# Kernel tuning notes

Hardware: AMD Instinct MI355X
Metric: run time of the kernel (lower is better)

The kernel has to match this reference:

```python
import jax, jax.numpy as jnp
from jax import lax
import numpy as np

NUM_TAGS = 128
BATCH = 256
SEQ = 1024


def setup_inputs() -> dict:
    key = jax.random.key(0)
    k1, k2, k3 = jax.random.split(key, 3)
    emissions = jax.random.normal(k1, (BATCH, SEQ, NUM_TAGS), dtype=jnp.float32)
    tags = jax.random.randint(k2, (BATCH, SEQ), 0, NUM_TAGS)
    mask = jnp.ones((BATCH, SEQ), dtype=jnp.float32)
    # xavier_uniform on [K,K] then clamp to [-1,1]
    limit = float(np.sqrt(6.0 / (NUM_TAGS + NUM_TAGS)))
    transitions = jnp.clip(
        jax.random.uniform(k3, (NUM_TAGS, NUM_TAGS), minval=-limit, maxval=limit),
        -1.0, 1.0).astype(jnp.float32)
    return {"emissions": emissions, "transitions": transitions, "tags": tags, "mask": mask}


def _log_partition(emissions, transitions, mask):
    # emissions: [B,S,K], mask: [B,S]
    alpha0 = emissions[:, 0]  # [B,K]
    emit_ts = jnp.swapaxes(emissions[:, 1:], 0, 1)  # [S-1,B,K]
    mask_ts = jnp.swapaxes(mask[:, 1:], 0, 1)       # [S-1,B]

    def step(alpha, xs):
        emit_t, mask_t = xs
        # [B,K,1] + [1,K,K] + [B,1,K] -> logsumexp over prev-tag axis
        new = jax.nn.logsumexp(alpha[:, :, None] + transitions[None, :, :] + emit_t[:, None, :], axis=1)
        alpha = jnp.where(mask_t[:, None].astype(bool), new, alpha)
        return alpha, None

    alpha, _ = lax.scan(step, alpha0, (emit_ts, mask_ts))
    return jax.nn.logsumexp(alpha, axis=1)  # [B]


def reference(emissions, transitions, tags, mask):
    # gold-path score
    emit_score = jnp.take_along_axis(emissions, tags[:, :, None], axis=2)[:, :, 0]  # [B,S]
    score = (emit_score * mask).sum(axis=1)
    trans_scores = transitions[tags[:, :-1], tags[:, 1:]] * mask[:, 1:]
    score = score + trans_scores.sum(axis=1)
    logZ = _log_partition(emissions, transitions, mask)
    return (logZ - score).mean()
```

## Files before the change

kernel.cpp:

```cpp
#include <hip/hip_runtime.h>
#include <stdint.h>

#define SEQ      1024
#define NT       128
#define NBATCH   256
#define MID      512
#define WS_STRIDE 132

#if defined(__has_builtin)
#if __has_builtin(__builtin_amdgcn_fdot2_f32_bf16)
#define HAVE_BF16_DOT2 1
#endif
#endif

#ifdef HAVE_BF16_DOT2
typedef __bf16 v2bf __attribute__((ext_vector_type(2)));
#define DOT2ACC(a, su, wu) \
    a = __builtin_amdgcn_fdot2_f32_bf16(__builtin_bit_cast(v2bf, (su)), \
                                        __builtin_bit_cast(v2bf, (wu)), a, false)
#else
#define DOT2ACC(a, su, wu) { \
    a = fmaf(__uint_as_float((wu) << 16),         __uint_as_float((su) << 16),         a); \
    a = fmaf(__uint_as_float((wu) & 0xffff0000u), __uint_as_float((su) & 0xffff0000u), a); }
#endif

#define RALL(X) X(0) X(1) X(2) X(3) X(4) X(5) X(6) X(7) \
                X(8) X(9) X(10) X(11) X(12) X(13) X(14) X(15)
#define DECLW(k) uint32_t W##k;
#define INITW(k) { \
    float f0_ = __expf(wbase[(2 * (k)    ) * wstr]); \
    float f1_ = __expf(wbase[(2 * (k) + 1) * wstr]); \
    asm("v_cvt_pk_bf16_f32 %0, %1, %2" : "=v"(W##k) : "v"(f0_), "v"(f1_)); }
#define PINW(k)  asm volatile("" : "+v"(W##k));

#define MQ(c, k0, k1, k2, k3) { \
    uint4 u_ = *(const uint4*)(gp + 4 * (c)); \
    DOT2ACC(a0, u_.x, W##k0); \
    DOT2ACC(a1, u_.y, W##k1); \
    DOT2ACC(a2, u_.z, W##k2); \
    DOT2ACC(a3, u_.w, W##k3); }

#define MATVEC32(S_) { \
    float a0 = 0.f, a1 = 0.f, a2 = 0.f, a3 = 0.f; \
    MQ(0,0,1,2,3) MQ(1,4,5,6,7) MQ(2,8,9,10,11) MQ(3,12,13,14,15) \
    S_ = (a0 + a1) + (a2 + a3); \
    S_ += __shfl_xor(S_, 1, 64); \
    S_ += __shfl_xor(S_, 2, 64); }

#define BF16_STORE(buf_, val_) { \
    uint32_t pk_; \
    asm("v_cvt_pk_bf16_f32 %0, %1, %2" : "=v"(pk_) : "v"(val_), "v"(val_)); \
    ((unsigned short*)(buf_))[jt] = (unsigned short)(pk_ & 0xffffu); }

__global__ __launch_bounds__(512) void crf_chains(
    const float* __restrict__ emissions,
    const float* __restrict__ transitions,
    const int*   __restrict__ tags,
    const float* __restrict__ mask,
    float* __restrict__ out,
    float* __restrict__ ws)
{
    const int blk = blockIdx.x;
    const int tid = threadIdx.x;

    if (blk >= 2 * NBATCH) {
        int b    = (blk - 2 * NBATCH) * 8 + (tid >> 6);
        int lane = tid & 63;
        const float* emb = emissions + (size_t)b * SEQ * NT;
        const int*   tgb = tags + (size_t)b * SEQ;
        const float* mkb = mask + (size_t)b * SEQ;
        float sc = 0.f;
        for (int t = lane; t < SEQ; t += 64) {
            int   tg = tgb[t];
            float mt = mkb[t];
            sc += emb[t * NT + tg] * mt;
            if (t >= 1) sc += transitions[tgb[t - 1] * NT + tg] * mt;
        }
#pragma unroll
        for (int o = 32; o > 0; o >>= 1) sc += __shfl_down(sc, o, 64);
        if (lane == 0) atomicAdd(out, -sc * (1.0f / NBATCH));
        return;
    }

    __shared__ __align__(16) uint32_t buf[2][NT / 2];

    const int jt = tid >> 2;
    const int q  = tid & 3;

    const bool fwd = (blk < NBATCH);
    const int  b   = fwd ? blk : blk - NBATCH;

    const float* emb = emissions + (size_t)b * SEQ * NT;
    const float* mkb = mask + (size_t)b * SEQ;

    const float* wbase = fwd ? (transitions + (size_t)(32 * q) * NT + jt)
                             : (transitions + (size_t)jt * NT + 32 * q);
    const int    wstr  = fwd ? NT : 1;

    RALL(DECLW)
    RALL(INITW)
    RALL(PINW)

    int   kSum = 0, p = 0;
    float gcur = 0.f, beta = 1.0f;
    float E0, E1, M0, M1;

    if (fwd) {
        gcur = __expf(emb[jt]);
        if (q == 0) BF16_STORE(buf[0], gcur);
        E0 = emb[1 * NT + jt];  E1 = emb[2 * NT + jt];
        M0 = mkb[1];            M1 = mkb[2];
    } else {
        float w0 = __expf(emb[(size_t)(SEQ - 1) * NT + jt]);
        if (q == 0) BF16_STORE(buf[0], w0);
        E0 = emb[(size_t)(SEQ - 2) * NT + jt];
        E1 = emb[(size_t)(SEQ - 3) * NT + jt];
        M0 = mkb[SEQ - 1];      M1 = mkb[SEQ - 2];
    }
    __syncthreads();

    if (fwd) {
        for (int s = 0; s < MID; ++s) {
            float En = emb[(size_t)(3 + s) * NT + jt];
            float Mn = mkb[3 + s];
            if (M0 != 0.0f) {
                const uint32_t* gp = buf[p] + 16 * q;
                uint32_t anchor = buf[p][0];
                float sres;
                MATVEC32(sres);
                int   e  = (int)((anchor >> 7) & 0xff);
                float rc = __uint_as_float((uint32_t)(254 - e) << 23);
                kSum += e - 127;
                if (q == 0) {
                    gcur = sres * rc * __expf(E0);
                    BF16_STORE(buf[p ^ 1], gcur);
                }
                p ^= 1;
            }
            __syncthreads();
            E0 = E1; E1 = En; M0 = M1; M1 = Mn;
        }
        float* wsb = ws + (size_t)b * WS_STRIDE;
        if (q == 0)  wsb[jt] = gcur;
        if (tid == 0) wsb[128] = (float)kSum;
    } else {
        for (int s = 0; s < MID - 1; ++s) {
            float En = emb[(size_t)(SEQ - 4 - s) * NT + jt];
            float Mn = mkb[SEQ - 3 - s];
            {
                const uint32_t* gp = buf[p] + 16 * q;
                uint32_t anchor = buf[p][0];
                float sres;
                MATVEC32(sres);
                int   e  = (int)((anchor >> 7) & 0xff);
                float rc = __uint_as_float((uint32_t)(254 - e) << 23);
                kSum += e - 127;
                float bn = (M0 != 0.0f) ? sres * rc : beta * rc;
                beta = bn;
                if (q == 0) {
                    float g = bn * __expf(E0);
                    BF16_STORE(buf[p ^ 1], g);
                }
                p ^= 1;
            }
            __syncthreads();
            E0 = E1; E1 = En; M0 = M1; M1 = Mn;
        }
        float* wsb = ws + (size_t)(NBATCH + b) * WS_STRIDE;
        if (q == 0)  wsb[jt] = beta;
        if (tid == 0) wsb[128] = (float)kSum;
    }
}

__global__ __launch_bounds__(64) void crf_combine(
    const float* __restrict__ ws, float* __restrict__ out)
{
    int b    = blockIdx.x;
    int lane = threadIdx.x;
    const float* af = ws + (size_t)b * WS_STRIDE;
    const float* bf = ws + (size_t)(NBATCH + b) * WS_STRIDE;
    float d = af[lane] * bf[lane] + af[lane + 64] * bf[lane + 64];
#pragma unroll
    for (int o = 32; o > 0; o >>= 1) d += __shfl_down(d, o, 64);
    if (lane == 0) {
        float logZ = __logf(d) + (af[128] + bf[128]) * 0.69314718055994531f;
        atomicAdd(out, logZ * (1.0f / NBATCH));
    }
}

extern "C" void kernel_launch(void* const* d_in, const int* in_sizes, int n_in,
                              void* d_out, int out_size, void* d_ws, size_t ws_size,
                              hipStream_t stream) {
    const float* emissions   = (const float*)d_in[0];
    const float* transitions = (const float*)d_in[1];
    const int*   tags        = (const int*)d_in[2];
    const float* mask        = (const float*)d_in[3];
    float*       out         = (float*)d_out;
    float*       ws          = (float*)d_ws;

    hipMemsetAsync(out, 0, sizeof(float), stream);
    crf_chains<<<2 * NBATCH + 32, 512, 0, stream>>>(
        emissions, transitions, tags, mask, out, ws);
    crf_combine<<<NBATCH, 64, 0, stream>>>(ws, out);
}
```

Before: 252.7 us.

## Process four batch chains per block to amortize barriers and transition registers

Each block now advances four independent batch recurrences in lockstep, so one barrier per step and one register-resident copy of the transition matrix are shared by four chains. This raises instruction-level parallelism within each step and cuts the block count from 512 to 128 chain blocks. The bf16 dot2 builtin is also replaced unconditionally with a manual two-FMA expansion, which doubles the arithmetic instructions in the matvec. The risks are fewer blocks than compute units (underfilling the GPU) and a longer serial critical path per block.

```diff
diff --git a/kernel.cpp b/kernel.cpp
--- a/kernel.cpp
+++ b/kernel.cpp
@@ -6,23 +6,7 @@
 #define NBATCH   256
 #define MID      512
 #define WS_STRIDE 132
-
-#if defined(__has_builtin)
-#if __has_builtin(__builtin_amdgcn_fdot2_f32_bf16)
-#define HAVE_BF16_DOT2 1
-#endif
-#endif
-
-#ifdef HAVE_BF16_DOT2
-typedef __bf16 v2bf __attribute__((ext_vector_type(2)));
-#define DOT2ACC(a, su, wu) \
-    a = __builtin_amdgcn_fdot2_f32_bf16(__builtin_bit_cast(v2bf, (su)), \
-                                        __builtin_bit_cast(v2bf, (wu)), a, false)
-#else
-#define DOT2ACC(a, su, wu) { \
-    a = fmaf(__uint_as_float((wu) << 16),         __uint_as_float((su) << 16),         a); \
-    a = fmaf(__uint_as_float((wu) & 0xffff0000u), __uint_as_float((su) & 0xffff0000u), a); }
-#endif
+#define NB4      4
 
 #define RALL(X) X(0) X(1) X(2) X(3) X(4) X(5) X(6) X(7) \
                 X(8) X(9) X(10) X(11) X(12) X(13) X(14) X(15)
@@ -33,6 +17,10 @@
     asm("v_cvt_pk_bf16_f32 %0, %1, %2" : "=v"(W##k) : "v"(f0_), "v"(f1_)); }
 #define PINW(k)  asm volatile("" : "+v"(W##k));
 
+#define DOT2ACC(a, su, wu) { \
+    a = fmaf(__uint_as_float((wu) << 16),         __uint_as_float((su) << 16),         a); \
+    a = fmaf(__uint_as_float((wu) & 0xffff0000u), __uint_as_float((su) & 0xffff0000u), a); }
+
 #define MQ(c, k0, k1, k2, k3) { \
     uint4 u_ = *(const uint4*)(gp + 4 * (c)); \
     DOT2ACC(a0, u_.x, W##k0); \
@@ -47,10 +35,10 @@
     S_ += __shfl_xor(S_, 1, 64); \
     S_ += __shfl_xor(S_, 2, 64); }
 
-#define BF16_STORE(buf_, val_) { \
+#define BF16_STORE(bufp_, val_) { \
     uint32_t pk_; \
     asm("v_cvt_pk_bf16_f32 %0, %1, %2" : "=v"(pk_) : "v"(val_), "v"(val_)); \
-    ((unsigned short*)(buf_))[jt] = (unsigned short)(pk_ & 0xffffu); }
+    ((unsigned short*)(bufp_))[jt] = (unsigned short)(pk_ & 0xffffu); }
 
 __global__ __launch_bounds__(512) void crf_chains(
     const float* __restrict__ emissions,
@@ -63,8 +51,8 @@
     const int blk = blockIdx.x;
     const int tid = threadIdx.x;
 
-    if (blk >= 2 * NBATCH) {
-        int b    = (blk - 2 * NBATCH) * 8 + (tid >> 6);
+    if (blk >= 2 * (NBATCH / NB4)) {
+        int b    = (blk - 2 * (NBATCH / NB4)) * 8 + (tid >> 6);
         int lane = tid & 63;
         const float* emb = emissions + (size_t)b * SEQ * NT;
         const int*   tgb = tags + (size_t)b * SEQ;
@@ -82,16 +70,13 @@
         return;
     }
 
-    __shared__ __align__(16) uint32_t buf[2][NT / 2];
+    __shared__ __align__(16) uint32_t buf[2][NB4][NT / 2];
 
     const int jt = tid >> 2;
     const int q  = tid & 3;
 
-    const bool fwd = (blk < NBATCH);
-    const int  b   = fwd ? blk : blk - NBATCH;
-
-    const float* emb = emissions + (size_t)b * SEQ * NT;
-    const float* mkb = mask + (size_t)b * SEQ;
+    const bool fwd = (blk < NBATCH / NB4);
+    const int  b0  = (fwd ? blk : blk - NBATCH / NB4) * NB4;
 
     const float* wbase = fwd ? (transitions + (size_t)(32 * q) * NT + jt)
                              : (transitions + (size_t)jt * NT + 32 * q);
@@ -101,74 +86,99 @@
     RALL(INITW)
     RALL(PINW)
 
-    int   kSum = 0, p = 0;
-    float gcur = 0.f, beta = 1.0f;
-    float E0, E1, M0, M1;
-
-    if (fwd) {
-        gcur = __expf(emb[jt]);
-        if (q == 0) BF16_STORE(buf[0], gcur);
-        E0 = emb[1 * NT + jt];  E1 = emb[2 * NT + jt];
-        M0 = mkb[1];            M1 = mkb[2];
-    } else {
-        float w0 = __expf(emb[(size_t)(SEQ - 1) * NT + jt]);
-        if (q == 0) BF16_STORE(buf[0], w0);
-        E0 = emb[(size_t)(SEQ - 2) * NT + jt];
-        E1 = emb[(size_t)(SEQ - 3) * NT + jt];
-        M0 = mkb[SEQ - 1];      M1 = mkb[SEQ - 2];
+    const float* embi[NB4];
+    const float* mkbi[NB4];
+#pragma unroll
+    for (int i = 0; i < NB4; ++i) {
+        embi[i] = emissions + (size_t)(b0 + i) * SEQ * NT;
+        mkbi[i] = mask + (size_t)(b0 + i) * SEQ;
+    }
+
+    int   kSum[NB4] = {0, 0, 0, 0};
+    int   pb[NB4]   = {0, 0, 0, 0};
+    float gcur[NB4], beta[NB4];
+    float E0[NB4], E1[NB4], M0[NB4], M1[NB4];
+
+#pragma unroll
+    for (int i = 0; i < NB4; ++i) {
+        beta[i] = 1.0f;
+        if (fwd) {
+            gcur[i] = __expf(embi[i][jt]);
+            if (q == 0) BF16_STORE(buf[0][i], gcur[i]);
+            E0[i] = embi[i][1 * NT + jt];  E1[i] = embi[i][2 * NT + jt];
+            M0[i] = mkbi[i][1];            M1[i] = mkbi[i][2];
+        } else {
+            float w0 = __expf(embi[i][(size_t)(SEQ - 1) * NT + jt]);
+            if (q == 0) BF16_STORE(buf[0][i], w0);
+            E0[i] = embi[i][(size_t)(SEQ - 2) * NT + jt];
+            E1[i] = embi[i][(size_t)(SEQ - 3) * NT + jt];
+            M0[i] = mkbi[i][SEQ - 1];      M1[i] = mkbi[i][SEQ - 2];
+        }
     }
     __syncthreads();
 
     if (fwd) {
         for (int s = 0; s < MID; ++s) {
-            float En = emb[(size_t)(3 + s) * NT + jt];
-            float Mn = mkb[3 + s];
-            if (M0 != 0.0f) {
-                const uint32_t* gp = buf[p] + 16 * q;
-                uint32_t anchor = buf[p][0];
-                float sres;
-                MATVEC32(sres);
-                int   e  = (int)((anchor >> 7) & 0xff);
-                float rc = __uint_as_float((uint32_t)(254 - e) << 23);
-                kSum += e - 127;
-                if (q == 0) {
-                    gcur = sres * rc * __expf(E0);
-                    BF16_STORE(buf[p ^ 1], gcur);
+#pragma unroll
+            for (int i = 0; i < NB4; ++i) {
+                float En = embi[i][(size_t)(3 + s) * NT + jt];
+                float Mn = mkbi[i][3 + s];
+                if (M0[i] != 0.0f) {
+                    const uint32_t* gp = buf[pb[i]][i] + 16 * q;
+                    uint32_t anchor = buf[pb[i]][i][0];
+                    float sres;
+                    MATVEC32(sres);
+                    int   e  = (int)((anchor >> 7) & 0xff);
+                    float rc = __uint_as_float((uint32_t)(254 - e) << 23);
+                    kSum[i] += e - 127;
+                    if (q == 0) {
+                        gcur[i] = sres * rc * __expf(E0[i]);
+                        BF16_STORE(buf[pb[i] ^ 1][i], gcur[i]);
+                    }
+                    pb[i] ^= 1;
                 }
-                p ^= 1;
+                E0[i] = E1[i]; E1[i] = En; M0[i] = M1[i]; M1[i] = Mn;
             }
             __syncthreads();
-            E0 = E1; E1 = En; M0 = M1; M1 = Mn;
-        }
-        float* wsb = ws + (size_t)b * WS_STRIDE;
-        if (q == 0)  wsb[jt] = gcur;
-        if (tid == 0) wsb[128] = (float)kSum;
+        }
+#pragma unroll
+        for (int i = 0; i < NB4; ++i) {
+            float* wsb = ws + (size_t)(b0 + i) * WS_STRIDE;
+            if (q == 0)  wsb[jt] = gcur[i];
+            if (tid == 0) wsb[128] = (float)kSum[i];
+        }
     } else {
         for (int s = 0; s < MID - 1; ++s) {
-            float En = emb[(size_t)(SEQ - 4 - s) * NT + jt];
-            float Mn = mkb[SEQ - 3 - s];
-            {
-                const uint32_t* gp = buf[p] + 16 * q;
-                uint32_t anchor = buf[p][0];
-                float sres;
-                MATVEC32(sres);
-                int   e  = (int)((anchor >> 7) & 0xff);
-                float rc = __uint_as_float((uint32_t)(254 - e) << 23);
-                kSum += e - 127;
-                float bn = (M0 != 0.0f) ? sres * rc : beta * rc;
-                beta = bn;
-                if (q == 0) {
-                    float g = bn * __expf(E0);
-                    BF16_STORE(buf[p ^ 1], g);
+#pragma unroll
+            for (int i = 0; i < NB4; ++i) {
+                float En = embi[i][(size_t)(SEQ - 4 - s) * NT + jt];
+                float Mn = mkbi[i][SEQ - 3 - s];
+                {
+                    const uint32_t* gp = buf[pb[i]][i] + 16 * q;
+                    uint32_t anchor = buf[pb[i]][i][0];
+                    float sres;
+                    MATVEC32(sres);
+                    int   e  = (int)((anchor >> 7) & 0xff);
+                    float rc = __uint_as_float((uint32_t)(254 - e) << 23);
+                    kSum[i] += e - 127;
+                    float bn = (M0[i] != 0.0f) ? sres * rc : beta[i] * rc;
+                    beta[i] = bn;
+                    if (q == 0) {
+                        float g = bn * __expf(E0[i]);
+                        BF16_STORE(buf[pb[i] ^ 1][i], g);
+                    }
+                    pb[i] ^= 1;
                 }
-                p ^= 1;
+                E0[i] = E1[i]; E1[i] = En; M0[i] = M1[i]; M1[i] = Mn;
             }
             __syncthreads();
-            E0 = E1; E1 = En; M0 = M1; M1 = Mn;
-        }
-        float* wsb = ws + (size_t)(NBATCH + b) * WS_STRIDE;
-        if (q == 0)  wsb[jt] = beta;
-        if (tid == 0) wsb[128] = (float)kSum;
+        }
+#pragma unroll
+        for (int i = 0; i < NB4; ++i) {
+            float* wsb = ws + (size_t)(NBATCH + b0 + i) * WS_STRIDE;
+            if (q == 0)  wsb[jt] = beta[i];
+            if (tid == 0) wsb[128] = (float)kSum[i];
+        }
     }
 }
 
@@ -199,7 +209,7 @@
     float*       ws          = (float*)d_ws;
 
     hipMemsetAsync(out, 0, sizeof(float), stream);
-    crf_chains<<<2 * NBATCH + 32, 512, 0, stream>>>(
+    crf_chains<<<2 * (NBATCH / NB4) + 32, 512, 0, stream>>>(
         emissions, transitions, tags, mask, out, ws);
     crf_combine<<<NBATCH, 64, 0, stream>>>(ws, out);
 }
```

Measured after the change: 796.9 us. 3.15x slower.

## Rescale every fourth step, use a lighter LDS barrier, drop the bf16 dot2 intrinsic

Applied to the files above, without the earlier changes.

The forward and backward scaled recurrences now renormalise by the anchor exponent only on every fourth step, which removes an LDS read and some scalar work from most iterations of the serial chain. __syncthreads is replaced by an inline s_waitcnt lgkmcnt(0) plus s_barrier, so the barrier waits only on LDS traffic and not on the global prefetch loads. The bf16 dot2 intrinsic path is removed and the dot product always uses two fp32 FMAs, which doubles the ALU instructions in the matvec. Skipping rescales lets values drift by up to about four steps' growth before correction, which fp32 should tolerate.

```diff
diff --git a/kernel.cpp b/kernel.cpp
--- a/kernel.cpp
+++ b/kernel.cpp
@@ -7,22 +7,11 @@
 #define MID      512
 #define WS_STRIDE 132
 
-#if defined(__has_builtin)
-#if __has_builtin(__builtin_amdgcn_fdot2_f32_bf16)
-#define HAVE_BF16_DOT2 1
-#endif
-#endif
-
-#ifdef HAVE_BF16_DOT2
-typedef __bf16 v2bf __attribute__((ext_vector_type(2)));
-#define DOT2ACC(a, su, wu) \
-    a = __builtin_amdgcn_fdot2_f32_bf16(__builtin_bit_cast(v2bf, (su)), \
-                                        __builtin_bit_cast(v2bf, (wu)), a, false)
-#else
+#define BARRIER() asm volatile("s_waitcnt lgkmcnt(0)\n\ts_barrier" ::: "memory")
+
 #define DOT2ACC(a, su, wu) { \
     a = fmaf(__uint_as_float((wu) << 16),         __uint_as_float((su) << 16),         a); \
     a = fmaf(__uint_as_float((wu) & 0xffff0000u), __uint_as_float((su) & 0xffff0000u), a); }
-#endif
 
 #define RALL(X) X(0) X(1) X(2) X(3) X(4) X(5) X(6) X(7) \
                 X(8) X(9) X(10) X(11) X(12) X(13) X(14) X(15)
@@ -47,10 +36,10 @@
     S_ += __shfl_xor(S_, 1, 64); \
     S_ += __shfl_xor(S_, 2, 64); }
 
-#define BF16_STORE(buf_, val_) { \
+#define BF16_STORE(bufp_, val_) { \
     uint32_t pk_; \
     asm("v_cvt_pk_bf16_f32 %0, %1, %2" : "=v"(pk_) : "v"(val_), "v"(val_)); \
-    ((unsigned short*)(buf_))[jt] = (unsigned short)(pk_ & 0xffffu); }
+    ((unsigned short*)(bufp_))[jt] = (unsigned short)(pk_ & 0xffffu); }
 
 __global__ __launch_bounds__(512) void crf_chains(
     const float* __restrict__ emissions,
@@ -123,21 +112,25 @@
         for (int s = 0; s < MID; ++s) {
             float En = emb[(size_t)(3 + s) * NT + jt];
             float Mn = mkb[3 + s];
+            const bool resc = ((s & 3) == 3);
             if (M0 != 0.0f) {
                 const uint32_t* gp = buf[p] + 16 * q;
-                uint32_t anchor = buf[p][0];
+                float rc = 1.0f;
+                if (resc) {
+                    uint32_t anchor = buf[p][0];
+                    int e = (int)((anchor >> 7) & 0xff);
+                    rc = __uint_as_float((uint32_t)(254 - e) << 23);
+                    kSum += e - 127;
+                }
                 float sres;
                 MATVEC32(sres);
-                int   e  = (int)((anchor >> 7) & 0xff);
-                float rc = __uint_as_float((uint32_t)(254 - e) << 23);
-                kSum += e - 127;
                 if (q == 0) {
                     gcur = sres * rc * __expf(E0);
                     BF16_STORE(buf[p ^ 1], gcur);
                 }
                 p ^= 1;
             }
-            __syncthreads();
+            BARRIER();
             E0 = E1; E1 = En; M0 = M1; M1 = Mn;
         }
         float* wsb = ws + (size_t)b * WS_STRIDE;
@@ -147,14 +140,18 @@
         for (int s = 0; s < MID - 1; ++s) {
             float En = emb[(size_t)(SEQ - 4 - s) * NT + jt];
             float Mn = mkb[SEQ - 3 - s];
+            const bool resc = ((s & 3) == 3);
             {
                 const uint32_t* gp = buf[p] + 16 * q;
-                uint32_t anchor = buf[p][0];
+                float rc = 1.0f;
+                if (resc) {
+                    uint32_t anchor = buf[p][0];
+                    int e = (int)((anchor >> 7) & 0xff);
+                    rc = __uint_as_float((uint32_t)(254 - e) << 23);
+                    kSum += e - 127;
+                }
                 float sres;
                 MATVEC32(sres);
-                int   e  = (int)((anchor >> 7) & 0xff);
-                float rc = __uint_as_float((uint32_t)(254 - e) << 23);
-                kSum += e - 127;
                 float bn = (M0 != 0.0f) ? sres * rc : beta * rc;
                 beta = bn;
                 if (q == 0) {
@@ -163,7 +160,7 @@
                 }
                 p ^= 1;
             }
-            __syncthreads();
+            BARRIER();
             E0 = E1; E1 = En; M0 = M1; M1 = Mn;
         }
         float* wsb = ws + (size_t)(NBATCH + b) * WS_STRIDE;
```

Measured after the change: 317.5 us. +25.7%, slower.
